# Performance work log

Hardware: AMD Instinct MI355X
Metric: run time of the kernel (lower is better)

The kernel has to match this reference:

```python
import jax, jax.numpy as jnp
import numpy as np

T_THR = 2.0   # temperature for threshold softmax over teachers
T_KD = 20.0   # KD temperature
ALPHA = 0.8   # KD mixing coefficient


def setup_inputs() -> dict:
    key = jax.random.key(0)
    ks = jax.random.split(key, 10)
    B, C = 4096, 1000
    d = {f"outputs{i+1}": jax.random.normal(ks[i], (B, C), dtype=jnp.float32) for i in range(8)}
    d["out_s"] = jax.random.normal(ks[8], (B, C), dtype=jnp.float32)
    d["targets"] = jax.random.randint(ks[9], (B,), 0, C, dtype=jnp.int64)
    return d


def reference(outputs1, outputs2, outputs3, outputs4, outputs5, outputs6, outputs7, outputs8, out_s, targets):
    outs = jnp.stack([outputs1, outputs2, outputs3, outputs4,
                      outputs5, outputs6, outputs7, outputs8])      # [8,B,C]
    mimic = outs.mean(axis=0)                                       # [B,C]
    all9 = jnp.concatenate([outs, mimic[None]], axis=0)             # [9,B,C]

    # per-(teacher,sample) top-2 margin, zero if target is not the argmax
    top2, _ = jax.lax.top_k(all9, 2)                                # [9,B,2]
    tgt_logit = jnp.take_along_axis(all9, targets[None, :, None], axis=2)[..., 0]  # [9,B]
    margin = jnp.where(tgt_logit == top2[..., 0], top2[..., 0] - top2[..., 1], 0.0)  # [9,B]
    thr = jax.nn.softmax(margin / T_THR, axis=0)                    # [9,B] softmax over 9 teachers

    max_preds = outs.max()                                          # scalar over the 8 teachers

    # cross-entropy of student (same for every teacher branch)
    logp_s = jax.nn.log_softmax(out_s, axis=-1)                     # [B,C]
    CE = -jnp.take_along_axis(logp_s, targets[:, None], axis=1)[:, 0]  # [B]

    # KD term per teacher
    logp_sT = jax.nn.log_softmax(out_s / T_KD, axis=-1)             # [B,C]
    p_tT = jax.nn.softmax(all9 / T_KD, axis=-1)                     # [9,B,C]
    KD = -jnp.sum(p_tT * logp_sT[None], axis=-1) * (T_KD * T_KD)    # [9,B]

    # dynamic per-sample weights
    w = tgt_logit / max_preds                                       # [9,B]
    loss = (1.0 - ALPHA * w) * CE[None] + ALPHA * w * KD            # [9,B]

    return jnp.sum(thr * loss, axis=0).mean()
```

## Files before the change

kernel.cpp:

```cpp
#include <hip/hip_runtime.h>

constexpr int   B        = 4096;
constexpr int   C        = 1000;
constexpr float ALPHA    = 0.8f;
constexpr float INV_TKD  = 0.05f;
constexpr float TKD2     = 400.0f;
constexpr float INV_TTHR = 0.5f;
constexpr float SENT     = -1e30f;

__global__ __launch_bounds__(256) void row_kernel(
    const float* __restrict__ T0, const float* __restrict__ T1,
    const float* __restrict__ T2, const float* __restrict__ T3,
    const float* __restrict__ T4, const float* __restrict__ T5,
    const float* __restrict__ T6, const float* __restrict__ T7,
    const float* __restrict__ S,  const int* __restrict__ TGT,
    float* __restrict__ ws_ce, float* __restrict__ ws_g, float* __restrict__ ws_m)
{
    const int lane = threadIdx.x & 63;
    const int wid  = threadIdx.x >> 6;
    const int b    = blockIdx.x * 4 + wid;
    const size_t base = (size_t)b * C;

    const int tgt   = TGT[b];
    const int uidx  = ((tgt >> 8) << 2) | (tgt & 3);
    const int slane = (tgt >> 2) & 63;

    auto load_row = [&](const float* __restrict__ p, float (&v)[16]) {
        const float4* p4 = (const float4*)(p + base);
#pragma unroll
        for (int k = 0; k < 4; ++k) {
            if (k < 3 || lane < 58) {
                float4 f = p4[lane + 64 * k];
                v[4*k+0] = f.x; v[4*k+1] = f.y; v[4*k+2] = f.z; v[4*k+3] = f.w;
            } else {
                v[4*k+0] = SENT; v[4*k+1] = SENT; v[4*k+2] = SENT; v[4*k+3] = SENT;
            }
        }
    };

    auto extract = [&](const float (&v)[16]) -> float {
        float cand = 0.0f;
#pragma unroll
        for (int i = 0; i < 16; ++i) cand = (i == uidx) ? v[i] : cand;
        return __shfl(cand, slane, 64);
    };

    float sv[16];
    load_row(S, sv);

    float smax = SENT;
#pragma unroll
    for (int i = 0; i < 16; ++i) smax = fmaxf(smax, sv[i]);
#pragma unroll
    for (int m = 1; m < 64; m <<= 1) smax = fmaxf(smax, __shfl_xor(smax, m, 64));

#pragma unroll
    for (int i = 0; i < 16; ++i) sv[i] -= smax;

    float z1 = 0.0f, zT = 0.0f;
#pragma unroll
    for (int i = 0; i < 16; ++i) {
        z1 += __expf(sv[i]);
        zT += __expf(sv[i] * INV_TKD);
    }
#pragma unroll
    for (int m = 1; m < 64; m <<= 1) {
        z1 += __shfl_xor(z1, m, 64);
        zT += __shfl_xor(zT, m, 64);
    }
    const float logZ1 = __logf(z1);
    const float logZT = __logf(zT);
    const float sd_tgt = extract(sv);
    const float ce = logZ1 - sd_tgt;

    float acc[16];
#pragma unroll
    for (int i = 0; i < 16; ++i) acc[i] = 0.0f;

    float rowmax8 = SENT;
    float mx = 0.0f, s1 = 0.0f, s2 = 0.0f;

    auto process_vals = [&](const float (&v)[16]) -> float {
        float m1 = SENT, m2 = SENT;
#pragma unroll
        for (int i = 0; i < 16; ++i) {
            float x = v[i];
            if (x > m1) { m2 = m1; m1 = x; } else { m2 = fmaxf(m2, x); }
        }
#pragma unroll
        for (int m = 1; m < 64; m <<= 1) {
            float o1 = __shfl_xor(m1, m, 64);
            float o2 = __shfl_xor(m2, m, 64);
            float n1 = fmaxf(m1, o1);
            float n2 = fmaxf(fminf(m1, o1), (m1 >= o1) ? m2 : o2);
            m1 = n1; m2 = n2;
        }
        const float tval = extract(v);

        float Z = 0.0f, Ssum = 0.0f;
#pragma unroll
        for (int i = 0; i < 16; ++i) {
            float e = __expf((v[i] - m1) * INV_TKD);
            Z    += e;
            Ssum += e * sv[i];
        }
#pragma unroll
        for (int m = 1; m < 64; m <<= 1) {
            Z    += __shfl_xor(Z, m, 64);
            Ssum += __shfl_xor(Ssum, m, 64);
        }

        const float kd = TKD2 * (logZT - INV_TKD * (Ssum / Z));
        const float margin = (tval == m1) ? (m1 - m2) : 0.0f;
        const float u = tval * (kd - ce);

        const float nmx = fmaxf(mx, margin);
        const float sc  = __expf((mx - nmx) * INV_TTHR);
        const float ee  = __expf((margin - nmx) * INV_TTHR);
        s1 = s1 * sc + ee;
        s2 = s2 * sc + ee * u;
        mx = nmx;
        return m1;
    };

    auto process_teacher = [&](const float* __restrict__ p) {
        float v[16];
        load_row(p, v);
#pragma unroll
        for (int i = 0; i < 16; ++i) acc[i] += v[i];
        rowmax8 = fmaxf(rowmax8, process_vals(v));
    };

    process_teacher(T0); process_teacher(T1); process_teacher(T2); process_teacher(T3);
    process_teacher(T4); process_teacher(T5); process_teacher(T6); process_teacher(T7);

#pragma unroll
    for (int i = 0; i < 16; ++i) acc[i] *= 0.125f;
    process_vals(acc);

    if (lane == 0) {
        ws_ce[b] = ce;
        ws_g[b]  = s2 / s1;
        ws_m[b]  = rowmax8;
    }
}

__global__ __launch_bounds__(256) void fin_kernel(
    const float* __restrict__ ce, const float* __restrict__ g,
    const float* __restrict__ m, float* __restrict__ out)
{
    __shared__ float  smax[256];
    __shared__ double ssum[256];
    const int tid = threadIdx.x;

    float mx = SENT;
    for (int i = tid; i < B; i += 256) mx = fmaxf(mx, m[i]);
    smax[tid] = mx;
    __syncthreads();
    for (int s = 128; s > 0; s >>= 1) {
        if (tid < s) smax[tid] = fmaxf(smax[tid], smax[tid + s]);
        __syncthreads();
    }
    const float scale = ALPHA / smax[0];

    double acc = 0.0;
    for (int i = tid; i < B; i += 256) acc += (double)(ce[i] + g[i] * scale);
    ssum[tid] = acc;
    __syncthreads();
    for (int s = 128; s > 0; s >>= 1) {
        if (tid < s) ssum[tid] += ssum[tid + s];
        __syncthreads();
    }
    if (tid == 0) out[0] = (float)(ssum[0] * (1.0 / (double)B));
}

extern "C" void kernel_launch(void* const* d_in, const int* in_sizes, int n_in,
                              void* d_out, int out_size, void* d_ws, size_t ws_size,
                              hipStream_t stream)
{
    const float* T0 = (const float*)d_in[0];
    const float* T1 = (const float*)d_in[1];
    const float* T2 = (const float*)d_in[2];
    const float* T3 = (const float*)d_in[3];
    const float* T4 = (const float*)d_in[4];
    const float* T5 = (const float*)d_in[5];
    const float* T6 = (const float*)d_in[6];
    const float* T7 = (const float*)d_in[7];
    const float* S  = (const float*)d_in[8];
    const int*   TG = (const int*)d_in[9];

    float* ws = (float*)d_ws;
    float* ws_ce = ws;
    float* ws_g  = ws + B;
    float* ws_m  = ws + 2 * B;

    row_kernel<<<B / 4, 256, 0, stream>>>(T0, T1, T2, T3, T4, T5, T6, T7,
                                          S, TG, ws_ce, ws_g, ws_m);
    fin_kernel<<<1, 256, 0, stream>>>(ws_ce, ws_g, ws_m, (float*)d_out);
}
```

Measured before the change: 184.7 us.

## Map one row per block with cross-wave LDS reductions and prefetch next teacher

Switches from one wavefront per row to one 256-thread block per row, with each thread holding one float4 of every row. Reductions now combine wave-level shuffles with shared-memory partials and __syncthreads, and the next teacher row is loaded while the current one is processed. The aim is to cut register pressure, raise occupancy (launch bounds 256,8) and keep more memory requests in flight. In exchange the kernel adds many block-wide barriers per row, and the finalize kernel grows to 1024 threads.

```diff
diff --git a/kernel.cpp b/kernel.cpp
--- a/kernel.cpp
+++ b/kernel.cpp
@@ -8,7 +8,7 @@
 constexpr float INV_TTHR = 0.5f;
 constexpr float SENT     = -1e30f;
 
-__global__ __launch_bounds__(256) void row_kernel(
+__global__ __launch_bounds__(256, 8) void row_kernel(
     const float* __restrict__ T0, const float* __restrict__ T1,
     const float* __restrict__ T2, const float* __restrict__ T3,
     const float* __restrict__ T4, const float* __restrict__ T5,
@@ -16,77 +16,41 @@
     const float* __restrict__ S,  const int* __restrict__ TGT,
     float* __restrict__ ws_ce, float* __restrict__ ws_g, float* __restrict__ ws_m)
 {
-    const int lane = threadIdx.x & 63;
-    const int wid  = threadIdx.x >> 6;
-    const int b    = blockIdx.x * 4 + wid;
+    const int tid  = threadIdx.x;
+    const int lane = tid & 63;
+    const int wid  = tid >> 6;
+    const int b    = blockIdx.x;
     const size_t base = (size_t)b * C;
-
-    const int tgt   = TGT[b];
-    const int uidx  = ((tgt >> 8) << 2) | (tgt & 3);
-    const int slane = (tgt >> 2) & 63;
-
-    auto load_row = [&](const float* __restrict__ p, float (&v)[16]) {
-        const float4* p4 = (const float4*)(p + base);
-#pragma unroll
-        for (int k = 0; k < 4; ++k) {
-            if (k < 3 || lane < 58) {
-                float4 f = p4[lane + 64 * k];
-                v[4*k+0] = f.x; v[4*k+1] = f.y; v[4*k+2] = f.z; v[4*k+3] = f.w;
-            } else {
-                v[4*k+0] = SENT; v[4*k+1] = SENT; v[4*k+2] = SENT; v[4*k+3] = SENT;
-            }
-        }
-    };
-
-    auto extract = [&](const float (&v)[16]) -> float {
-        float cand = 0.0f;
-#pragma unroll
-        for (int i = 0; i < 16; ++i) cand = (i == uidx) ? v[i] : cand;
-        return __shfl(cand, slane, 64);
-    };
-
-    float sv[16];
-    load_row(S, sv);
-
-    float smax = SENT;
-#pragma unroll
-    for (int i = 0; i < 16; ++i) smax = fmaxf(smax, sv[i]);
-#pragma unroll
-    for (int m = 1; m < 64; m <<= 1) smax = fmaxf(smax, __shfl_xor(smax, m, 64));
-
-#pragma unroll
-    for (int i = 0; i < 16; ++i) sv[i] -= smax;
-
-    float z1 = 0.0f, zT = 0.0f;
-#pragma unroll
-    for (int i = 0; i < 16; ++i) {
-        z1 += __expf(sv[i]);
-        zT += __expf(sv[i] * INV_TKD);
-    }
-#pragma unroll
-    for (int m = 1; m < 64; m <<= 1) {
-        z1 += __shfl_xor(z1, m, 64);
-        zT += __shfl_xor(zT, m, 64);
-    }
-    const float logZ1 = __logf(z1);
-    const float logZT = __logf(zT);
-    const float sd_tgt = extract(sv);
-    const float ce = logZ1 - sd_tgt;
-
-    float acc[16];
-#pragma unroll
-    for (int i = 0; i < 16; ++i) acc[i] = 0.0f;
-
-    float rowmax8 = SENT;
-    float mx = 0.0f, s1 = 0.0f, s2 = 0.0f;
-
-    auto process_vals = [&](const float (&v)[16]) -> float {
-        float m1 = SENT, m2 = SENT;
-#pragma unroll
-        for (int i = 0; i < 16; ++i) {
-            float x = v[i];
-            if (x > m1) { m2 = m1; m1 = x; } else { m2 = fmaxf(m2, x); }
-        }
+    const bool valid = (tid < 250);
+
+    const int tgt  = TGT[b];
+    const int oc4  = tgt >> 2;
+    const int slot = tgt & 3;
+
+    __shared__ float red1a[9][4], red1b[9][4];
+    __shared__ float red2a[9][4], red2b[9][4];
+    __shared__ float tvs[9];
+    __shared__ float sredm[4], sred1[4], sredT[4];
+    __shared__ float stv;
+
+    auto load_row = [&](const float* __restrict__ p, float (&v)[4]) {
+        if (valid) {
+            float4 f = ((const float4*)(p + base))[tid];
+            v[0] = f.x; v[1] = f.y; v[2] = f.z; v[3] = f.w;
+        } else {
+            v[0] = SENT; v[1] = SENT; v[2] = SENT; v[3] = SENT;
+        }
+    };
+
+    auto wreduce_sum2 = [&](float& a, float& c) {
+#pragma unroll
+        for (int m = 1; m < 64; m <<= 1) {
+            a += __shfl_xor(a, m, 64);
+            c += __shfl_xor(c, m, 64);
+        }
+    };
+
+    auto wreduce_top2 = [&](float& m1, float& m2) {
 #pragma unroll
         for (int m = 1; m < 64; m <<= 1) {
             float o1 = __shfl_xor(m1, m, 64);
@@ -95,22 +59,76 @@
             float n2 = fmaxf(fminf(m1, o1), (m1 >= o1) ? m2 : o2);
             m1 = n1; m2 = n2;
         }
-        const float tval = extract(v);
-
-        float Z = 0.0f, Ssum = 0.0f;
-#pragma unroll
-        for (int i = 0; i < 16; ++i) {
-            float e = __expf((v[i] - m1) * INV_TKD);
-            Z    += e;
-            Ssum += e * sv[i];
-        }
-#pragma unroll
-        for (int m = 1; m < 64; m <<= 1) {
-            Z    += __shfl_xor(Z, m, 64);
-            Ssum += __shfl_xor(Ssum, m, 64);
-        }
-
-        const float kd = TKD2 * (logZT - INV_TKD * (Ssum / Z));
+    };
+
+    float sv[4];
+    load_row(S, sv);
+    float v[4];
+    load_row(T0, v);
+
+    float smax = fmaxf(fmaxf(sv[0], sv[1]), fmaxf(sv[2], sv[3]));
+#pragma unroll
+    for (int m = 1; m < 64; m <<= 1) smax = fmaxf(smax, __shfl_xor(smax, m, 64));
+    if (lane == 0) sredm[wid] = smax;
+    __syncthreads();
+    smax = fmaxf(fmaxf(sredm[0], sredm[1]), fmaxf(sredm[2], sredm[3]));
+
+#pragma unroll
+    for (int i = 0; i < 4; ++i) sv[i] -= smax;
+
+    float z1 = 0.0f, zT = 0.0f;
+#pragma unroll
+    for (int i = 0; i < 4; ++i) {
+        z1 += __expf(sv[i]);
+        zT += __expf(sv[i] * INV_TKD);
+    }
+    wreduce_sum2(z1, zT);
+    if (lane == 0) { sred1[wid] = z1; sredT[wid] = zT; }
+    if (tid == oc4) stv = sv[slot];
+    __syncthreads();
+    z1 = sred1[0] + sred1[1] + sred1[2] + sred1[3];
+    zT = sredT[0] + sredT[1] + sredT[2] + sredT[3];
+    const float logZ1 = __logf(z1);
+    const float logZT = __logf(zT);
+    const float ce = logZ1 - stv;
+
+    float acc[4] = {0.0f, 0.0f, 0.0f, 0.0f};
+    float rowmax8 = SENT;
+    float mx = 0.0f, s1 = 0.0f, s2 = 0.0f;
+
+    auto process = [&](const float (&w)[4], int br) -> float {
+        float h1 = fmaxf(w[0], w[1]), l1 = fminf(w[0], w[1]);
+        float h2 = fmaxf(w[2], w[3]), l2 = fminf(w[2], w[3]);
+        float m1 = fmaxf(h1, h2);
+        float m2 = fmaxf(fminf(h1, h2), (h1 >= h2) ? l1 : l2);
+        wreduce_top2(m1, m2);
+        if (lane == 0) { red1a[br][wid] = m1; red1b[br][wid] = m2; }
+        if (tid == oc4) tvs[br] = w[slot];
+        __syncthreads();
+        m1 = red1a[br][0]; m2 = red1b[br][0];
+#pragma unroll
+        for (int k = 1; k < 4; ++k) {
+            float a1 = red1a[br][k], a2 = red1b[br][k];
+            float n1 = fmaxf(m1, a1);
+            float n2 = fmaxf(fminf(m1, a1), (m1 >= a1) ? m2 : a2);
+            m1 = n1; m2 = n2;
+        }
+        const float tval = tvs[br];
+
+        float Z = 0.0f, Ss = 0.0f;
+#pragma unroll
+        for (int i = 0; i < 4; ++i) {
+            float e = __expf((w[i] - m1) * INV_TKD);
+            Z  += e;
+            Ss += e * sv[i];
+        }
+        wreduce_sum2(Z, Ss);
+        if (lane == 0) { red2a[br][wid] = Z; red2b[br][wid] = Ss; }
+        __syncthreads();
+        Z  = red2a[br][0] + red2a[br][1] + red2a[br][2] + red2a[br][3];
+        Ss = red2b[br][0] + red2b[br][1] + red2b[br][2] + red2b[br][3];
+
+        const float kd = TKD2 * (logZT - INV_TKD * (Ss / Z));
         const float margin = (tval == m1) ? (m1 - m2) : 0.0f;
         const float u = tval * (kd - ce);
 
@@ -123,51 +141,55 @@
         return m1;
     };
 
-    auto process_teacher = [&](const float* __restrict__ p) {
-        float v[16];
-        load_row(p, v);
-#pragma unroll
-        for (int i = 0; i < 16; ++i) acc[i] += v[i];
-        rowmax8 = fmaxf(rowmax8, process_vals(v));
-    };
-
-    process_teacher(T0); process_teacher(T1); process_teacher(T2); process_teacher(T3);
-    process_teacher(T4); process_teacher(T5); process_teacher(T6); process_teacher(T7);
-
-#pragma unroll
-    for (int i = 0; i < 16; ++i) acc[i] *= 0.125f;
-    process_vals(acc);
-
-    if (lane == 0) {
+    const float* Tp[8] = {T0, T1, T2, T3, T4, T5, T6, T7};
+    float vn[4];
+#pragma unroll
+    for (int t = 0; t < 8; ++t) {
+        if (t < 7) load_row(Tp[t + 1], vn);
+#pragma unroll
+        for (int i = 0; i < 4; ++i) acc[i] += v[i];
+        rowmax8 = fmaxf(rowmax8, process(v, t));
+        if (t < 7) {
+#pragma unroll
+            for (int i = 0; i < 4; ++i) v[i] = vn[i];
+        }
+    }
+
+    float mv[4];
+#pragma unroll
+    for (int i = 0; i < 4; ++i) mv[i] = acc[i] * 0.125f;
+    process(mv, 8);
+
+    if (tid == 0) {
         ws_ce[b] = ce;
         ws_g[b]  = s2 / s1;
         ws_m[b]  = rowmax8;
     }
 }
 
-__global__ __launch_bounds__(256) void fin_kernel(
+__global__ __launch_bounds__(1024) void fin_kernel(
     const float* __restrict__ ce, const float* __restrict__ g,
     const float* __restrict__ m, float* __restrict__ out)
 {
-    __shared__ float  smax[256];
-    __shared__ double ssum[256];
+    __shared__ float  smax[1024];
+    __shared__ double ssum[1024];
     const int tid = threadIdx.x;
 
     float mx = SENT;
-    for (int i = tid; i < B; i += 256) mx = fmaxf(mx, m[i]);
+    for (int i = tid; i < B; i += 1024) mx = fmaxf(mx, m[i]);
     smax[tid] = mx;
     __syncthreads();
-    for (int s = 128; s > 0; s >>= 1) {
+    for (int s = 512; s > 0; s >>= 1) {
         if (tid < s) smax[tid] = fmaxf(smax[tid], smax[tid + s]);
         __syncthreads();
     }
     const float scale = ALPHA / smax[0];
 
     double acc = 0.0;
-    for (int i = tid; i < B; i += 256) acc += (double)(ce[i] + g[i] * scale);
+    for (int i = tid; i < B; i += 1024) acc += (double)(ce[i] + g[i] * scale);
     ssum[tid] = acc;
     __syncthreads();
-    for (int s = 128; s > 0; s >>= 1) {
+    for (int s = 512; s > 0; s >>= 1) {
         if (tid < s) ssum[tid] += ssum[tid + s];
         __syncthreads();
     }
@@ -194,7 +216,7 @@
     float* ws_g  = ws + B;
     float* ws_m  = ws + 2 * B;
 
-    row_kernel<<<B / 4, 256, 0, stream>>>(T0, T1, T2, T3, T4, T5, T6, T7,
-                                          S, TG, ws_ce, ws_g, ws_m);
-    fin_kernel<<<1, 256, 0, stream>>>(ws_ce, ws_g, ws_m, (float*)d_out);
+    row_kernel<<<B, 256, 0, stream>>>(T0, T1, T2, T3, T4, T5, T6, T7,
+                                      S, TG, ws_ce, ws_g, ws_m);
+    fin_kernel<<<1, 1024, 0, stream>>>(ws_ce, ws_g, ws_m, (float*)d_out);
 }
```

Measured after the change: 325.7 us. 76.3% more time.
